# Kernel tuning notes

Measured on AMD Instinct MI355X. Metric: run time of the kernel, lower is better.

The kernel has to match this reference:

```python
import jax, jax.numpy as jnp
import numpy as np

N_ROWS = 600000
D_FEAT = 128
N_SEG = 50000


def setup_inputs() -> dict:
    key = jax.random.key(0)
    kx, ki = jax.random.split(key)
    x = jax.random.normal(kx, (N_ROWS, D_FEAT), dtype=jnp.float32)
    index = jnp.sort(jax.random.randint(ki, (N_ROWS,), 0, N_SEG, dtype=jnp.int32))
    # pin max id so output segment count is exactly N_SEG (static shape)
    index = index.at[-1].set(N_SEG - 1)
    return {"x": x, "index": index}


def reference(x, index):
    # tf.math.segment_sum(x, index): sum rows of x grouped by sorted segment id.
    # Output shape: [N_SEG, D_FEAT]
    return jax.ops.segment_sum(x, index.reshape(-1), num_segments=N_SEG,
                               indices_are_sorted=True)
```

## Files before the change

kernel.cpp:

```cpp
#include <hip/hip_runtime.h>

#define N_ROWS 600000
#define D_FEAT 128
#define N_SEG 50000

__global__ __launch_bounds__(256) void seg_offsets_kernel(
    const int* __restrict__ idx, int* __restrict__ offsets) {
    int r = blockIdx.x * 256 + threadIdx.x;
    if (r >= N_ROWS) return;
    int cur = idx[r];
    int prev = (r == 0) ? -1 : idx[r - 1];
    for (int s = prev + 1; s <= cur; ++s) offsets[s] = r;
    if (r == N_ROWS - 1)
        for (int s = cur + 1; s <= N_SEG; ++s) offsets[s] = N_ROWS;
}

__global__ __launch_bounds__(256) void SegmentSum_20272245637565_kernel(
    const float* __restrict__ x, const int* __restrict__ offsets,
    float* __restrict__ out) {
    const int wave = threadIdx.x >> 6;
    const int lane = threadIdx.x & 63;
    const int seg  = blockIdx.x * 4 + wave;

    const int start = offsets[seg];
    const int end   = offsets[seg + 1];

    const float2* __restrict__ x2 = reinterpret_cast<const float2*>(x);

    float2 a0{0.f, 0.f}, a1{0.f, 0.f}, a2{0.f, 0.f}, a3{0.f, 0.f};
    int r = start;
    for (; r + 4 <= end; r += 4) {
        float2 v0 = x2[(long)(r + 0) * 64 + lane];
        float2 v1 = x2[(long)(r + 1) * 64 + lane];
        float2 v2 = x2[(long)(r + 2) * 64 + lane];
        float2 v3 = x2[(long)(r + 3) * 64 + lane];
        a0.x += v0.x; a0.y += v0.y;
        a1.x += v1.x; a1.y += v1.y;
        a2.x += v2.x; a2.y += v2.y;
        a3.x += v3.x; a3.y += v3.y;
    }
    for (; r < end; ++r) {
        float2 v = x2[(long)r * 64 + lane];
        a0.x += v.x; a0.y += v.y;
    }
    float2 acc;
    acc.x = (a0.x + a1.x) + (a2.x + a3.x);
    acc.y = (a0.y + a1.y) + (a2.y + a3.y);
    reinterpret_cast<float2*>(out)[(long)seg * 64 + lane] = acc;
}

extern "C" void kernel_launch(void* const* d_in, const int* in_sizes, int n_in,
                              void* d_out, int out_size, void* d_ws, size_t ws_size,
                              hipStream_t stream) {
    const float* x  = (const float*)d_in[0];
    const int* idx  = (const int*)d_in[1];
    float* out      = (float*)d_out;
    int* offsets    = (int*)d_ws;

    seg_offsets_kernel<<<(N_ROWS + 255) / 256, 256, 0, stream>>>(idx, offsets);
    SegmentSum_20272245637565_kernel<<<N_SEG / 4, 256, 0, stream>>>(x, offsets, out);
}
```

Baseline: 68.74 us.

## Fuse offset computation into segment sum with row-chunked wave ownership

Drops the separate offsets kernel. Each wave now owns a 64-row chunk, finds segment starts in its chunk with a ballot, and sums every segment that begins there, reading ahead into later chunks when a segment runs past the chunk end. Empty segments are zero-filled by the wave that sees the gap. This removes one kernel launch and the offsets round trip, and spreads work by rows instead of by segments. In exchange, waves whose segments cross chunk boundaries do longer serial loops, and the last wave zero-fills the tail alone.

```diff
diff --git a/kernel.cpp b/kernel.cpp
--- a/kernel.cpp
+++ b/kernel.cpp
@@ -3,33 +3,15 @@
 #define N_ROWS 600000
 #define D_FEAT 128
 #define N_SEG 50000
+#define CHUNK 64
+#define NCHUNK (N_ROWS / CHUNK)
 
-__global__ __launch_bounds__(256) void seg_offsets_kernel(
-    const int* __restrict__ idx, int* __restrict__ offsets) {
-    int r = blockIdx.x * 256 + threadIdx.x;
-    if (r >= N_ROWS) return;
-    int cur = idx[r];
-    int prev = (r == 0) ? -1 : idx[r - 1];
-    for (int s = prev + 1; s <= cur; ++s) offsets[s] = r;
-    if (r == N_ROWS - 1)
-        for (int s = cur + 1; s <= N_SEG; ++s) offsets[s] = N_ROWS;
-}
-
-__global__ __launch_bounds__(256) void SegmentSum_20272245637565_kernel(
-    const float* __restrict__ x, const int* __restrict__ offsets,
-    float* __restrict__ out) {
-    const int wave = threadIdx.x >> 6;
-    const int lane = threadIdx.x & 63;
-    const int seg  = blockIdx.x * 4 + wave;
-
-    const int start = offsets[seg];
-    const int end   = offsets[seg + 1];
-
-    const float2* __restrict__ x2 = reinterpret_cast<const float2*>(x);
-
-    float2 a0{0.f, 0.f}, a1{0.f, 0.f}, a2{0.f, 0.f}, a3{0.f, 0.f};
-    int r = start;
-    for (; r + 4 <= end; r += 4) {
+__device__ __forceinline__ void accum_rows(const float2* __restrict__ x2,
+                                           int rbeg, int rend, int lane,
+                                           float2& acc) {
+    float2 a0 = acc, a1{0.f, 0.f}, a2{0.f, 0.f}, a3{0.f, 0.f};
+    int r = rbeg;
+    for (; r + 4 <= rend; r += 4) {
         float2 v0 = x2[(long)(r + 0) * 64 + lane];
         float2 v1 = x2[(long)(r + 1) * 64 + lane];
         float2 v2 = x2[(long)(r + 2) * 64 + lane];
@@ -39,14 +21,66 @@
         a2.x += v2.x; a2.y += v2.y;
         a3.x += v3.x; a3.y += v3.y;
     }
-    for (; r < end; ++r) {
+    for (; r < rend; ++r) {
         float2 v = x2[(long)r * 64 + lane];
         a0.x += v.x; a0.y += v.y;
     }
-    float2 acc;
     acc.x = (a0.x + a1.x) + (a2.x + a3.x);
     acc.y = (a0.y + a1.y) + (a2.y + a3.y);
-    reinterpret_cast<float2*>(out)[(long)seg * 64 + lane] = acc;
+}
+
+__global__ __launch_bounds__(256) void SegmentSum_20272245637565_kernel(
+    const float* __restrict__ x, const int* __restrict__ idx,
+    float* __restrict__ out) {
+    const int wid = blockIdx.x * 4 + (threadIdx.x >> 6);
+    if (wid >= NCHUNK) return;
+    const int lane = threadIdx.x & 63;
+    const int base = wid * CHUNK;
+
+    const float2* __restrict__ x2 = reinterpret_cast<const float2*>(x);
+    float2* __restrict__ out2 = reinterpret_cast<float2*>(out);
+
+    int my = idx[base + lane];
+    int left = __shfl_up(my, 1, 64);
+    if (lane == 0) left = (base > 0) ? idx[base - 1] : -1;
+    unsigned long long starts = __ballot(my != left);
+
+    if (wid == NCHUNK - 1) {
+        int lastv = __shfl(my, 63, 64);
+        for (int e = lastv + 1; e < N_SEG; ++e)
+            out2[(long)e * 64 + lane] = make_float2(0.f, 0.f);
+    }
+    if (!starts) return;
+
+    int p = __ffsll(starts) - 1;
+    while (true) {
+        const int seg     = __shfl(my, p, 64);
+        const int prevSeg = __shfl(left, p, 64);
+        for (int e = prevSeg + 1; e < seg; ++e)
+            out2[(long)e * 64 + lane] = make_float2(0.f, 0.f);
+
+        unsigned long long rest = (p < 63) ? (starts >> (p + 1)) : 0ull;
+        float2 acc = make_float2(0.f, 0.f);
+        if (rest) {
+            const int nextp = p + 1 + (__ffsll(rest) - 1);
+            accum_rows(x2, base + p, base + nextp, lane, acc);
+            out2[(long)seg * 64 + lane] = acc;
+            p = nextp;
+        } else {
+            accum_rows(x2, base + p, base + CHUNK, lane, acc);
+            int nb = base + CHUNK;
+            while (nb < N_ROWS) {
+                int m2 = idx[nb + lane];
+                unsigned long long cont = __ballot(m2 == seg);
+                int cnt = (~cont) ? (__ffsll(~cont) - 1) : 64;
+                if (cnt > 0) accum_rows(x2, nb, nb + cnt, lane, acc);
+                if (cnt < 64) break;
+                nb += CHUNK;
+            }
+            out2[(long)seg * 64 + lane] = acc;
+            break;
+        }
+    }
 }
 
 extern "C" void kernel_launch(void* const* d_in, const int* in_sizes, int n_in,
@@ -55,8 +89,7 @@
     const float* x  = (const float*)d_in[0];
     const int* idx  = (const int*)d_in[1];
     float* out      = (float*)d_out;
-    int* offsets    = (int*)d_ws;
 
-    seg_offsets_kernel<<<(N_ROWS + 255) / 256, 256, 0, stream>>>(idx, offsets);
-    SegmentSum_20272245637565_kernel<<<N_SEG / 4, 256, 0, stream>>>(x, offsets, out);
+    const int nblocks = (NCHUNK + 3) / 4;
+    SegmentSum_20272245637565_kernel<<<nblocks, 256, 0, stream>>>(x, idx, out);
 }
```

Result: slower. 74.32 us (+8.1%).
